# Performance work log

Hardware: AMD Instinct MI355X
Metric: run time of the kernel (lower is better)

Reference implementation:

```python
import jax, jax.numpy as jnp
import numpy as np
from jax import lax

B, H, W = 64, 512, 512
KH, KW = 7, 7


def setup_inputs() -> dict:
    key = jax.random.key(0)
    k1, k2, k3 = jax.random.split(key, 3)
    enc_x = jax.random.normal(k1, (B, 1, H, W), dtype=jnp.float32)
    weight = jax.random.normal(k2, (1, 1, KH, KW), dtype=jnp.float32)
    bias = jax.random.normal(k3, (1,), dtype=jnp.float32)
    return {"enc_x": enc_x, "weight": weight, "bias": bias}


def reference(enc_x, weight, bias):
    # Plaintext math of the CKKS Conv2dFunction: stride-1 VALID 2D conv,
    # single input channel, single output channel, scalar bias.
    out = lax.conv_general_dilated(
        enc_x, weight,
        window_strides=(1, 1),
        padding="VALID",
        dimension_numbers=("NCHW", "OIHW", "NCHW"),
    )
    return out + bias.reshape(1, 1, 1, 1)
```

## Files before the change

kernel.cpp:

```cpp
#include <hip/hip_runtime.h>

#define HW 512
#define OW 506

template<int SH>
__device__ __forceinline__ void conv_rows(const float* __restrict__ p0,
                                          const float (&wv)[49],
                                          float (&acc)[16]) {
#pragma unroll
    for (int ir = 0; ir < 10; ++ir) {
        const float* p = p0 + ir * HW;
        const float4 q0 = *reinterpret_cast<const float4*>(p);
        const float4 q1 = *reinterpret_cast<const float4*>(p + 4);
        const float4 q2 = *reinterpret_cast<const float4*>(p + 8);
        const float f12[12] = {q0.x, q0.y, q0.z, q0.w,
                               q1.x, q1.y, q1.z, q1.w,
                               q2.x, q2.y, q2.z, q2.w};
#pragma unroll
        for (int kr = 0; kr < 7; ++kr) {
            const int s = ir - kr;
            if (s >= 0 && s < 4) {
#pragma unroll
                for (int kc = 0; kc < 7; ++kc) {
                    const float wk = wv[kr * 7 + kc];
#pragma unroll
                    for (int j = 0; j < 4; ++j)
                        acc[s * 4 + j] = fmaf(wk, f12[SH + kc + j], acc[s * 4 + j]);
                }
            }
        }
    }
}

__global__ __launch_bounds__(256) void conv7x7_v12(
    const float* __restrict__ in,
    const float* __restrict__ weight,
    const float* __restrict__ bias,
    float* __restrict__ out)
{
    const int tid  = threadIdx.x;
    const int lane = tid & 63;
    const int w    = tid >> 6;
    const int bx   = blockIdx.x;
    const int x0   = bx ? 250 : 0;
    const int y0   = min((int)blockIdx.y * 16, OW - 16);
    const int yb   = y0 + w * 4;
    const int b    = blockIdx.z;

    float wv[49];
#pragma unroll
    for (int i = 0; i < 49; ++i)
        wv[i] = __uint_as_float(__builtin_amdgcn_readfirstlane(__float_as_uint(weight[i])));
    const float bv = __uint_as_float(__builtin_amdgcn_readfirstlane(__float_as_uint(bias[0])));

    const float* __restrict__ ib = in + (size_t)b * (HW * HW);

    const int cb = x0 + 4 * lane;
    const float* p0 = ib + (size_t)yb * HW + (cb - (bx ? 2 : 0));

    float acc[16];
#pragma unroll
    for (int i = 0; i < 16; ++i) acc[i] = 0.f;

    if (bx == 0) conv_rows<0>(p0, wv, acc);
    else         conv_rows<2>(p0, wv, acc);

    float* __restrict__ outb = out + (size_t)b * (OW * OW);
#pragma unroll
    for (int s = 0; s < 4; ++s) {
        float* orow = outb + (size_t)(yb + s) * OW + cb;
        *reinterpret_cast<float2*>(orow) =
            make_float2(acc[s * 4 + 0] + bv, acc[s * 4 + 1] + bv);
        *reinterpret_cast<float2*>(orow + 2) =
            make_float2(acc[s * 4 + 2] + bv, acc[s * 4 + 3] + bv);
    }
}

extern "C" void kernel_launch(void* const* d_in, const int* in_sizes, int n_in,
                              void* d_out, int out_size, void* d_ws, size_t ws_size,
                              hipStream_t stream) {
    const float* enc_x  = (const float*)d_in[0];
    const float* weight = (const float*)d_in[1];
    const float* bias   = (const float*)d_in[2];
    float* outp         = (float*)d_out;

    dim3 grid(2, 32, 64);
    dim3 block(256);
    hipLaunchKernelGGL(conv7x7_v12, grid, block, 0, stream,
                       enc_x, weight, bias, outp);
}
```

Before: 38.89 us.

## Software-pipeline input row loads with inline asm and explicit vmcnt waits

```diff
diff --git a/kernel.cpp b/kernel.cpp
--- a/kernel.cpp
+++ b/kernel.cpp
@@ -3,36 +3,91 @@
 #define HW 512
 #define OW 506
 
+typedef float vf4 __attribute__((ext_vector_type(4)));
+
+#define LOAD_ROW(d0, d1, d2, addr, O0, O1, O2)                        \
+    asm volatile("global_load_dwordx4 %0, %3, off offset:" #O0 "\n\t" \
+                 "global_load_dwordx4 %1, %3, off offset:" #O1 "\n\t" \
+                 "global_load_dwordx4 %2, %3, off offset:" #O2        \
+                 : "=&v"(d0), "=&v"(d1), "=&v"(d2)                    \
+                 : "v"(addr) : "memory")
+
+#define WAIT_ROW(d0, d1, d2, N)                                       \
+    asm volatile("s_waitcnt vmcnt(" #N ")"                            \
+                 : "+v"(d0), "+v"(d1), "+v"(d2))
+
 template<int SH>
-__device__ __forceinline__ void conv_rows(const float* __restrict__ p0,
-                                          const float (&wv)[49],
-                                          float (&acc)[16]) {
+__device__ __forceinline__ void row_fma(int ir, const vf4 (&b)[3],
+                                        const float (&wv)[49],
+                                        float (&acc)[16]) {
 #pragma unroll
-    for (int ir = 0; ir < 10; ++ir) {
-        const float* p = p0 + ir * HW;
-        const float4 q0 = *reinterpret_cast<const float4*>(p);
-        const float4 q1 = *reinterpret_cast<const float4*>(p + 4);
-        const float4 q2 = *reinterpret_cast<const float4*>(p + 8);
-        const float f12[12] = {q0.x, q0.y, q0.z, q0.w,
-                               q1.x, q1.y, q1.z, q1.w,
-                               q2.x, q2.y, q2.z, q2.w};
+    for (int kr = 0; kr < 7; ++kr) {
+        const int s = ir - kr;
+        if (s >= 0 && s < 4) {
 #pragma unroll
-        for (int kr = 0; kr < 7; ++kr) {
-            const int s = ir - kr;
-            if (s >= 0 && s < 4) {
+            for (int kc = 0; kc < 7; ++kc) {
+                const float wk = wv[kr * 7 + kc];
 #pragma unroll
-                for (int kc = 0; kc < 7; ++kc) {
-                    const float wk = wv[kr * 7 + kc];
-#pragma unroll
-                    for (int j = 0; j < 4; ++j)
-                        acc[s * 4 + j] = fmaf(wk, f12[SH + kc + j], acc[s * 4 + j]);
+                for (int j = 0; j < 4; ++j) {
+                    const int e = SH + kc + j;
+                    acc[s * 4 + j] = fmaf(wk, b[e >> 2][e & 3], acc[s * 4 + j]);
                 }
             }
         }
     }
 }
 
-__global__ __launch_bounds__(256) void conv7x7_v12(
+template<int SH>
+__device__ __forceinline__ void conv_pipe(const float* __restrict__ p0,
+                                          const float (&wv)[49],
+                                          float (&acc)[16]) {
+    vf4 buf[4][3];
+    const float* a0 = p0;
+    const float* a1 = p0 + 2 * HW;
+    const float* a2 = p0 + 4 * HW;
+    const float* a3 = p0 + 6 * HW;
+    const float* a4 = p0 + 8 * HW;
+
+    LOAD_ROW(buf[0][0], buf[0][1], buf[0][2], a0, 0, 16, 32);
+    LOAD_ROW(buf[1][0], buf[1][1], buf[1][2], a0, 2048, 2064, 2080);
+    LOAD_ROW(buf[2][0], buf[2][1], buf[2][2], a1, 0, 16, 32);
+    LOAD_ROW(buf[3][0], buf[3][1], buf[3][2], a1, 2048, 2064, 2080);
+
+    WAIT_ROW(buf[0][0], buf[0][1], buf[0][2], 9);
+    row_fma<SH>(0, buf[0], wv, acc);
+    LOAD_ROW(buf[0][0], buf[0][1], buf[0][2], a2, 0, 16, 32);
+
+    WAIT_ROW(buf[1][0], buf[1][1], buf[1][2], 9);
+    row_fma<SH>(1, buf[1], wv, acc);
+    LOAD_ROW(buf[1][0], buf[1][1], buf[1][2], a2, 2048, 2064, 2080);
+
+    WAIT_ROW(buf[2][0], buf[2][1], buf[2][2], 9);
+    row_fma<SH>(2, buf[2], wv, acc);
+    LOAD_ROW(buf[2][0], buf[2][1], buf[2][2], a3, 0, 16, 32);
+
+    WAIT_ROW(buf[3][0], buf[3][1], buf[3][2], 9);
+    row_fma<SH>(3, buf[3], wv, acc);
+    LOAD_ROW(buf[3][0], buf[3][1], buf[3][2], a3, 2048, 2064, 2080);
+
+    WAIT_ROW(buf[0][0], buf[0][1], buf[0][2], 9);
+    row_fma<SH>(4, buf[0], wv, acc);
+    LOAD_ROW(buf[0][0], buf[0][1], buf[0][2], a4, 0, 16, 32);
+
+    WAIT_ROW(buf[1][0], buf[1][1], buf[1][2], 9);
+    row_fma<SH>(5, buf[1], wv, acc);
+    LOAD_ROW(buf[1][0], buf[1][1], buf[1][2], a4, 2048, 2064, 2080);
+
+    WAIT_ROW(buf[2][0], buf[2][1], buf[2][2], 9);
+    row_fma<SH>(6, buf[2], wv, acc);
+    WAIT_ROW(buf[3][0], buf[3][1], buf[3][2], 6);
+    row_fma<SH>(7, buf[3], wv, acc);
+    WAIT_ROW(buf[0][0], buf[0][1], buf[0][2], 3);
+    row_fma<SH>(8, buf[0], wv, acc);
+    WAIT_ROW(buf[1][0], buf[1][1], buf[1][2], 0);
+    row_fma<SH>(9, buf[1], wv, acc);
+}
+
+__global__ __launch_bounds__(256) void conv7x7_v16(
     const float* __restrict__ in,
     const float* __restrict__ weight,
     const float* __restrict__ bias,
@@ -62,8 +117,8 @@
 #pragma unroll
     for (int i = 0; i < 16; ++i) acc[i] = 0.f;
 
-    if (bx == 0) conv_rows<0>(p0, wv, acc);
-    else         conv_rows<2>(p0, wv, acc);
+    if (bx == 0) conv_pipe<0>(p0, wv, acc);
+    else         conv_pipe<2>(p0, wv, acc);
 
     float* __restrict__ outb = out + (size_t)b * (OW * OW);
 #pragma unroll
@@ -86,6 +141,6 @@
 
     dim3 grid(2, 32, 64);
     dim3 block(256);
-    hipLaunchKernelGGL(conv7x7_v12, grid, block, 0, stream,
+    hipLaunchKernelGGL(conv7x7_v16, grid, block, 0, stream,
                        enc_x, weight, bias, outp);
 }
```

Result: faster. 33.94 us (-12.7%).
